# Kernel tuning notes

Measured on AMD Instinct MI355X. Metric: run time of the kernel, lower is better.

## Reference

```python
import jax, jax.numpy as jnp
import numpy as np
from jax import lax

H = 32  # hidden size (hardcoded in the torch module)

def setup_inputs() -> dict:
    key = jax.random.key(0)
    ks = jax.random.split(key, 7)
    B, T, I = 2048, 512, 64
    s = 1.0 / np.sqrt(H)  # torch nn.LSTM default init scale
    return {
        "x": jax.random.normal(ks[0], (B, T, I), dtype=jnp.float32),
        "W_ih": jax.random.uniform(ks[1], (4 * H, I), jnp.float32, -s, s),
        "W_hh": jax.random.uniform(ks[2], (4 * H, H), jnp.float32, -s, s),
        "b_ih": jax.random.uniform(ks[3], (4 * H,), jnp.float32, -s, s),
        "b_hh": jax.random.uniform(ks[4], (4 * H,), jnp.float32, -s, s),
        "W_fc": jax.random.uniform(ks[5], (1, H), jnp.float32, -s, s),
        "b_fc": jax.random.uniform(ks[6], (1,), jnp.float32, -s, s),
    }

def _lstm_last_h(x, W_ih, W_hh, b_ih, b_hh):
    B = x.shape[0]
    # Precompute input projections for all timesteps: [B, T, 4H] -> [T, B, 4H]
    xg = jnp.einsum('bti,gi->btg', x, W_ih) + (b_ih + b_hh)
    xg = jnp.transpose(xg, (1, 0, 2))

    def step(carry, xt):
        h, c = carry
        g = xt + h @ W_hh.T  # [B, 4H]
        i = jax.nn.sigmoid(g[:, 0 * H:1 * H])
        f = jax.nn.sigmoid(g[:, 1 * H:2 * H])
        gg = jnp.tanh(g[:, 2 * H:3 * H])
        o = jax.nn.sigmoid(g[:, 3 * H:4 * H])
        c = f * c + i * gg
        h = o * jnp.tanh(c)
        return (h, c), None

    init = (jnp.zeros((B, H), x.dtype), jnp.zeros((B, H), x.dtype))
    (h, _), _ = lax.scan(step, init, xg)
    return h  # [B, H], last timestep hidden state

def reference(x, W_ih, W_hh, b_ih, b_hh, W_fc, b_fc):
    # Dropout is identity in eval mode; only the last timestep feeds fc.
    h = _lstm_last_h(x, W_ih, W_hh, b_ih, b_hh)
    return h @ W_fc.T + b_fc  # [B, 1]
```

## Files before the change

### kernel.cpp

```cpp
#include <hip/hip_runtime.h>

typedef __attribute__((ext_vector_type(8))) short short8;
typedef __attribute__((ext_vector_type(4))) float f32x4;

#define LOG2E 1.44269504088896340736f

__device__ __forceinline__ unsigned short f2bf(float f) {
    union { float f; unsigned u; } a; a.f = f;
    unsigned r = a.u + 0x7fffu + ((a.u >> 16) & 1u);
    return (unsigned short)(r >> 16);
}
__device__ __forceinline__ unsigned pk2(float x, float y) {
    return (unsigned)f2bf(x) | ((unsigned)f2bf(y) << 16);
}
__device__ __forceinline__ float sigm(float x) {
    return __builtin_amdgcn_rcpf(1.0f + __builtin_amdgcn_exp2f(-LOG2E * x));
}

__global__ __launch_bounds__(256, 2) void lstm_fused(
    const float* __restrict__ x,
    const float* __restrict__ Wih,
    const float* __restrict__ Whh,
    const float* __restrict__ bih,
    const float* __restrict__ bhh,
    const float* __restrict__ Wfc,
    const float* __restrict__ bfc,
    float* __restrict__ out)
{
    __shared__ unsigned short Wlds[128 * 80];
    __shared__ float xg_sh[4 * 16 * 132];

    const int tid  = threadIdx.x;
    const int lane = tid & 63;
    const int wv   = tid >> 6;
    const int b0   = blockIdx.x * 4 + wv;
    const int m    = lane & 15;
    const int quad = lane >> 4;
    const int cc   = lane & 31;

    {
        const float4* w4 = (const float4*)Wih;
        unsigned* wl = (unsigned*)Wlds;
        #pragma unroll
        for (int i = 0; i < 8; i++) {
            int fi = tid * 8 + i;
            int g  = fi >> 4;
            int k  = (fi & 15) << 2;
            float4 v = w4[fi];
            wl[g * 40 + (k >> 1) + 0] = pk2(v.x, v.y);
            wl[g * 40 + (k >> 1) + 1] = pk2(v.z, v.w);
        }
    }

    short8 Bh[8];
    #pragma unroll
    for (int t = 0; t < 8; t++) {
        const float4* wr = (const float4*)(Whh + (size_t)(16 * t + m) * 32 + quad * 8);
        float4 va = wr[0], vb = wr[1];
        union { short8 v; unsigned u[4]; } B;
        B.u[0] = pk2(va.x, va.y); B.u[1] = pk2(va.z, va.w);
        B.u[2] = pk2(vb.x, vb.y); B.u[3] = pk2(vb.z, vb.w);
        Bh[t] = B.v;
    }

    float biasv[8];
    #pragma unroll
    for (int n = 0; n < 8; n++) biasv[n] = bih[16 * n + m] + bhh[16 * n + m];

    const bool b4 = (lane & 16) != 0;
    const bool odd = (lane & 1) != 0;
    const int badr = quad * 32;

    __syncthreads();

    const float* xrow = x + ((size_t)b0 * 512 + m) * 64;
    float* xgw = xg_sh + wv * 2112;

    float c = 0.0f, h = 0.0f;
    int hpk = 0;
    const f32x4 z4 = {0.f, 0.f, 0.f, 0.f};

    float4 p0, p1, p2, p3;
    {
        const float4* r0 = (const float4*)xrow;
        p0 = r0[quad * 2];     p1 = r0[quad * 2 + 1];
        p2 = r0[8 + quad * 2]; p3 = r0[8 + quad * 2 + 1];
    }

    for (int ch = 0; ch < 32; ++ch) {
        union { short8 v; unsigned u[4]; } A0, A1;
        A0.u[0] = pk2(p0.x, p0.y); A0.u[1] = pk2(p0.z, p0.w);
        A0.u[2] = pk2(p1.x, p1.y); A0.u[3] = pk2(p1.z, p1.w);
        A1.u[0] = pk2(p2.x, p2.y); A1.u[1] = pk2(p2.z, p2.w);
        A1.u[2] = pk2(p3.x, p3.y); A1.u[3] = pk2(p3.z, p3.w);

        {
            const int chn = (ch < 31) ? ch + 1 : 31;
            const float4* n0 = (const float4*)(xrow + (size_t)chn * 1024);
            p0 = n0[quad * 2];     p1 = n0[quad * 2 + 1];
            p2 = n0[8 + quad * 2]; p3 = n0[8 + quad * 2 + 1];
        }

        #pragma unroll
        for (int n = 0; n < 8; n++) {
            const short8 B0 = *(const short8*)&Wlds[(16 * n + m) * 80 + quad * 8];
            const short8 B1 = *(const short8*)&Wlds[(16 * n + m) * 80 + 32 + quad * 8];
            f32x4 ar0 = {0.f, 0.f, 0.f, 0.f};
            ar0 = __builtin_amdgcn_mfma_f32_16x16x32_bf16(A0.v, B0, ar0, 0, 0, 0);
            ar0 = __builtin_amdgcn_mfma_f32_16x16x32_bf16(A1.v, B1, ar0, 0, 0, 0);
            const int pos = ((n & 1) << 6) + 4 * m + (n >> 1);
            #pragma unroll
            for (int r = 0; r < 4; r++) {
                xgw[(quad * 4 + r) * 132 + pos] = ar0[r] + biasv[n];
            }
        }

        #pragma unroll
        for (int tt = 0; tt < 16; ++tt) {
            union { short8 v; int u[4]; } abf;
            abf.u[0] = __builtin_amdgcn_ds_bpermute(badr,      hpk);
            abf.u[1] = __builtin_amdgcn_ds_bpermute(badr + 8,  hpk);
            abf.u[2] = __builtin_amdgcn_ds_bpermute(badr + 16, hpk);
            abf.u[3] = __builtin_amdgcn_ds_bpermute(badr + 24, hpk);

            const f32x4 a0 = __builtin_amdgcn_mfma_f32_16x16x32_bf16(abf.v, Bh[0], z4, 0, 0, 0);
            const f32x4 a1 = __builtin_amdgcn_mfma_f32_16x16x32_bf16(abf.v, Bh[1], z4, 0, 0, 0);
            const f32x4 a2 = __builtin_amdgcn_mfma_f32_16x16x32_bf16(abf.v, Bh[2], z4, 0, 0, 0);
            const f32x4 a3 = __builtin_amdgcn_mfma_f32_16x16x32_bf16(abf.v, Bh[3], z4, 0, 0, 0);
            const f32x4 a4 = __builtin_amdgcn_mfma_f32_16x16x32_bf16(abf.v, Bh[4], z4, 0, 0, 0);
            const f32x4 a5 = __builtin_amdgcn_mfma_f32_16x16x32_bf16(abf.v, Bh[5], z4, 0, 0, 0);
            const f32x4 a6 = __builtin_amdgcn_mfma_f32_16x16x32_bf16(abf.v, Bh[6], z4, 0, 0, 0);
            const f32x4 a7 = __builtin_amdgcn_mfma_f32_16x16x32_bf16(abf.v, Bh[7], z4, 0, 0, 0);
            const float hi = b4 ? a1[0] : a0[0];
            const float hf = b4 ? a3[0] : a2[0];
            const float hg = b4 ? a5[0] : a4[0];
            const float ho = b4 ? a7[0] : a6[0];

            const f32x4 xg4 = *(const f32x4*)&xgw[tt * 132 + 4 * cc];
            const float gi = xg4[0] + hi;
            const float gf = xg4[1] + hf;
            const float gg = xg4[2] + hg;
            const float go = xg4[3] + ho;

            const float iv = sigm(gi);
            const float fv = sigm(gf);
            const float gv = fmaf(2.0f, sigm(2.0f * gg), -1.0f);
            const float ov = sigm(go);
            c = fmaf(fv, c, iv * gv);
            const float th = fmaf(2.0f, sigm(2.0f * c), -1.0f);
            h = ov * th;

            const float hp = __shfl_xor(h, 1);
            const float hlo = odd ? hp : h;
            const float hhi = odd ? h : hp;
            hpk = (int)pk2(hlo, hhi);
        }
    }

    float p = h * Wfc[cc];
    #pragma unroll
    for (int msk = 16; msk >= 1; msk >>= 1) p += __shfl_xor(p, msk);
    if (lane == 0) out[b0] = p + bfc[0];
}

extern "C" void kernel_launch(void* const* d_in, const int* in_sizes, int n_in,
                              void* d_out, int out_size, void* d_ws, size_t ws_size,
                              hipStream_t stream) {
    const float* x   = (const float*)d_in[0];
    const float* Wih = (const float*)d_in[1];
    const float* Whh = (const float*)d_in[2];
    const float* bih = (const float*)d_in[3];
    const float* bhh = (const float*)d_in[4];
    const float* Wfc = (const float*)d_in[5];
    const float* bfc = (const float*)d_in[6];
    float* out = (float*)d_out;
    lstm_fused<<<dim3(512), dim3(256), 0, stream>>>(x, Wih, Whh, bih, bhh, Wfc, bfc, out);
}
```

Baseline: 459.7 us.

## Fold sigmoid scaling into weights, use hardware bf16 pack and DPP swap

Pre-scales the W_ih, W_hh and bias rows by -log2(e) (or -2log2(e) for the cell gate) so the per-step activation needs no multiply before exp2. The bias now enters as the MFMA accumulator init instead of a separate add. Software bf16 rounding is replaced by the v_cvt_pk_bf16_f32 instruction, and the neighbour-lane shuffle uses a DPP quad-permute instead of shfl_xor. The aim is to shorten the serial recurrence critical path. The scaled weights are rounded to bf16 after scaling, which slightly changes numerics.

```diff
diff --git a/kernel.cpp b/kernel.cpp
--- a/kernel.cpp
+++ b/kernel.cpp
@@ -4,17 +4,16 @@
 typedef __attribute__((ext_vector_type(4))) float f32x4;
 
 #define LOG2E 1.44269504088896340736f
+#define SC1 (-LOG2E)
+#define SC2 (-2.0f * LOG2E)
 
-__device__ __forceinline__ unsigned short f2bf(float f) {
-    union { float f; unsigned u; } a; a.f = f;
-    unsigned r = a.u + 0x7fffu + ((a.u >> 16) & 1u);
-    return (unsigned short)(r >> 16);
+__device__ __forceinline__ unsigned pkcvt(float lo, float hi) {
+    unsigned r;
+    asm("v_cvt_pk_bf16_f32 %0, %1, %2" : "=v"(r) : "v"(lo), "v"(hi));
+    return r;
 }
-__device__ __forceinline__ unsigned pk2(float x, float y) {
-    return (unsigned)f2bf(x) | ((unsigned)f2bf(y) << 16);
-}
-__device__ __forceinline__ float sigm(float x) {
-    return __builtin_amdgcn_rcpf(1.0f + __builtin_amdgcn_exp2f(-LOG2E * x));
+__device__ __forceinline__ float sige(float xpre) {
+    return __builtin_amdgcn_rcpf(1.0f + __builtin_amdgcn_exp2f(xpre));
 }
 
 __global__ __launch_bounds__(256, 2) void lstm_fused(
@@ -46,28 +45,34 @@
             int fi = tid * 8 + i;
             int g  = fi >> 4;
             int k  = (fi & 15) << 2;
+            const float s = ((g >> 5) == 2) ? SC2 : SC1;
             float4 v = w4[fi];
-            wl[g * 40 + (k >> 1) + 0] = pk2(v.x, v.y);
-            wl[g * 40 + (k >> 1) + 1] = pk2(v.z, v.w);
+            wl[g * 40 + (k >> 1) + 0] = pkcvt(v.x * s, v.y * s);
+            wl[g * 40 + (k >> 1) + 1] = pkcvt(v.z * s, v.w * s);
         }
     }
 
     short8 Bh[8];
     #pragma unroll
     for (int t = 0; t < 8; t++) {
+        const float s = ((t >> 1) == 2) ? SC2 : SC1;
         const float4* wr = (const float4*)(Whh + (size_t)(16 * t + m) * 32 + quad * 8);
         float4 va = wr[0], vb = wr[1];
         union { short8 v; unsigned u[4]; } B;
-        B.u[0] = pk2(va.x, va.y); B.u[1] = pk2(va.z, va.w);
-        B.u[2] = pk2(vb.x, vb.y); B.u[3] = pk2(vb.z, vb.w);
+        B.u[0] = pkcvt(va.x * s, va.y * s); B.u[1] = pkcvt(va.z * s, va.w * s);
+        B.u[2] = pkcvt(vb.x * s, vb.y * s); B.u[3] = pkcvt(vb.z * s, vb.w * s);
         Bh[t] = B.v;
     }
 
-    float biasv[8];
+    f32x4 Cb[8];
     #pragma unroll
-    for (int n = 0; n < 8; n++) biasv[n] = bih[16 * n + m] + bhh[16 * n + m];
+    for (int n = 0; n < 8; n++) {
+        const float s = ((n >> 1) == 2) ? SC2 : SC1;
+        const float b = s * (bih[16 * n + m] + bhh[16 * n + m]);
+        Cb[n][0] = b; Cb[n][1] = b; Cb[n][2] = b; Cb[n][3] = b;
+    }
 
-    const bool b4 = (lane & 16) != 0;
+    const bool b4  = (lane & 16) != 0;
     const bool odd = (lane & 1) != 0;
     const int badr = quad * 32;
 
@@ -77,7 +82,6 @@
     float* xgw = xg_sh + wv * 2112;
 
     float c = 0.0f, h = 0.0f;
-    int hpk = 0;
     const f32x4 z4 = {0.f, 0.f, 0.f, 0.f};
 
     float4 p0, p1, p2, p3;
@@ -89,10 +93,10 @@
 
     for (int ch = 0; ch < 32; ++ch) {
         union { short8 v; unsigned u[4]; } A0, A1;
-        A0.u[0] = pk2(p0.x, p0.y); A0.u[1] = pk2(p0.z, p0.w);
-        A0.u[2] = pk2(p1.x, p1.y); A0.u[3] = pk2(p1.z, p1.w);
-        A1.u[0] = pk2(p2.x, p2.y); A1.u[1] = pk2(p2.z, p2.w);
-        A1.u[2] = pk2(p3.x, p3.y); A1.u[3] = pk2(p3.z, p3.w);
+        A0.u[0] = pkcvt(p0.x, p0.y); A0.u[1] = pkcvt(p0.z, p0.w);
+        A0.u[2] = pkcvt(p1.x, p1.y); A0.u[3] = pkcvt(p1.z, p1.w);
+        A1.u[0] = pkcvt(p2.x, p2.y); A1.u[1] = pkcvt(p2.z, p2.w);
+        A1.u[2] = pkcvt(p3.x, p3.y); A1.u[3] = pkcvt(p3.z, p3.w);
 
         {
             const int chn = (ch < 31) ? ch + 1 : 31;
@@ -105,23 +109,29 @@
         for (int n = 0; n < 8; n++) {
             const short8 B0 = *(const short8*)&Wlds[(16 * n + m) * 80 + quad * 8];
             const short8 B1 = *(const short8*)&Wlds[(16 * n + m) * 80 + 32 + quad * 8];
-            f32x4 ar0 = {0.f, 0.f, 0.f, 0.f};
-            ar0 = __builtin_amdgcn_mfma_f32_16x16x32_bf16(A0.v, B0, ar0, 0, 0, 0);
-            ar0 = __builtin_amdgcn_mfma_f32_16x16x32_bf16(A1.v, B1, ar0, 0, 0, 0);
+            f32x4 ar0 = __builtin_amdgcn_mfma_f32_16x16x32_bf16(A0.v, B0, Cb[n], 0, 0, 0);
+            ar0       = __builtin_amdgcn_mfma_f32_16x16x32_bf16(A1.v, B1, ar0,   0, 0, 0);
             const int pos = ((n & 1) << 6) + 4 * m + (n >> 1);
             #pragma unroll
             for (int r = 0; r < 4; r++) {
-                xgw[(quad * 4 + r) * 132 + pos] = ar0[r] + biasv[n];
+                xgw[(quad * 4 + r) * 132 + pos] = ar0[r];
             }
         }
 
         #pragma unroll
         for (int tt = 0; tt < 16; ++tt) {
+            union { float f; int i; } hu; hu.f = h;
+            union { int i; float f; } hxu;
+            hxu.i = __builtin_amdgcn_mov_dpp(hu.i, 0xB1, 0xF, 0xF, true);
+            const unsigned pe = pkcvt(h, hxu.f);
+            const unsigned po = pkcvt(hxu.f, h);
+            const int pair = odd ? (int)po : (int)pe;
+
             union { short8 v; int u[4]; } abf;
-            abf.u[0] = __builtin_amdgcn_ds_bpermute(badr,      hpk);
-            abf.u[1] = __builtin_amdgcn_ds_bpermute(badr + 8,  hpk);
-            abf.u[2] = __builtin_amdgcn_ds_bpermute(badr + 16, hpk);
-            abf.u[3] = __builtin_amdgcn_ds_bpermute(badr + 24, hpk);
+            abf.u[0] = __builtin_amdgcn_ds_bpermute(badr,      pair);
+            abf.u[1] = __builtin_amdgcn_ds_bpermute(badr + 8,  pair);
+            abf.u[2] = __builtin_amdgcn_ds_bpermute(badr + 16, pair);
+            abf.u[3] = __builtin_amdgcn_ds_bpermute(badr + 24, pair);
 
             const f32x4 a0 = __builtin_amdgcn_mfma_f32_16x16x32_bf16(abf.v, Bh[0], z4, 0, 0, 0);
             const f32x4 a1 = __builtin_amdgcn_mfma_f32_16x16x32_bf16(abf.v, Bh[1], z4, 0, 0, 0);
@@ -137,23 +147,13 @@
             const float ho = b4 ? a7[0] : a6[0];
 
             const f32x4 xg4 = *(const f32x4*)&xgw[tt * 132 + 4 * cc];
-            const float gi = xg4[0] + hi;
-            const float gf = xg4[1] + hf;
-            const float gg = xg4[2] + hg;
-            const float go = xg4[3] + ho;
-
-            const float iv = sigm(gi);
-            const float fv = sigm(gf);
-            const float gv = fmaf(2.0f, sigm(2.0f * gg), -1.0f);
-            const float ov = sigm(go);
+            const float iv = sige(xg4[0] + hi);
+            const float fv = sige(xg4[1] + hf);
+            const float gv = fmaf(2.0f, sige(xg4[2] + hg), -1.0f);
+            const float ov = sige(xg4[3] + ho);
             c = fmaf(fv, c, iv * gv);
-            const float th = fmaf(2.0f, sigm(2.0f * c), -1.0f);
+            const float th = fmaf(2.0f, sige(c * SC2), -1.0f);
             h = ov * th;
-
-            const float hp = __shfl_xor(h, 1);
-            const float hlo = odd ? hp : h;
-            const float hhi = odd ? h : hp;
-            hpk = (int)pk2(hlo, hhi);
         }
     }
 
```

New measurement: 433.9 us. -5.6%, faster.
